# Optimization experiments

Measured on AMD Instinct MI355X. Metric: run time of the kernel, lower is better.

Reference implementation:

```python
import jax, jax.numpy as jnp
import numpy as np

HIDDEN = 128
HEADS = 8
HEAD_DIM = HIDDEN // HEADS
N = 2048
SCALE = HEAD_DIM ** -0.5


def setup_inputs() -> dict:
    key = jax.random.key(0)
    ks = jax.random.split(key, 12)
    # xavier_uniform bound for square (HIDDEN, HIDDEN) weights
    bound = float(np.sqrt(6.0 / (HIDDEN + HIDDEN)))
    def w(k):
        return jax.random.uniform(k, (HIDDEN, HIDDEN), jnp.float32, -bound, bound)
    return {
        "x": jax.random.normal(ks[0], (N, HIDDEN), jnp.float32),
        "attention_bias": jax.random.normal(ks[1], (N, N, HEADS), jnp.float32),
        "key_padding_mask": jnp.zeros((N,), jnp.bool_),
        "Wq": w(ks[2]), "bq": jnp.zeros((HIDDEN,), jnp.float32),
        "Wk": w(ks[3]), "bk": jnp.zeros((HIDDEN,), jnp.float32),
        "Wv": w(ks[4]), "bv": jnp.zeros((HIDDEN,), jnp.float32),
        "Wo": w(ks[5]), "bo": jnp.zeros((HIDDEN,), jnp.float32),
    }


def reference(x, attention_bias, key_padding_mask, Wq, bq, Wk, bk, Wv, bv, Wo, bo):
    n = x.shape[0]
    # torch Linear: y = x @ W.T + b
    q = (x @ Wq.T + bq).reshape(n, HEADS, HEAD_DIM).transpose(1, 0, 2)  # (H, N, D)
    k = (x @ Wk.T + bk).reshape(n, HEADS, HEAD_DIM).transpose(1, 0, 2)
    v = (x @ Wv.T + bv).reshape(n, HEADS, HEAD_DIM).transpose(1, 0, 2)
    scores = jnp.einsum('hnd,hmd->hnm', q, k) * SCALE        # (H, N, N)
    scores = scores + attention_bias.transpose(2, 0, 1)       # additive graph bias
    mask = key_padding_mask[None, None, :]                    # (1, 1, N) over keys
    scores = jnp.where(mask, -jnp.inf, scores)
    attn = jax.nn.softmax(scores, axis=-1)
    out = jnp.einsum('hnm,hmd->hnd', attn, v)                 # (H, N, D)
    out = out.transpose(1, 0, 2).reshape(n, HIDDEN)
    return out @ Wo.T + bo
```

## Files before the change

kernel.cpp:

```cpp
#include <hip/hip_runtime.h>
#include <hip/hip_bf16.h>

#define NSEQ 2048
#define HID 128
#define HEADS 8
#define HD 16
#define SCALE 0.25f
#define TQ 16
#define TK 64
#define SPLIT 8
#define KT_PER (NSEQ / TK / SPLIT)
#define QROW 160
#define PM_W 36
#define PH_W (16 * PM_W + 4)

typedef unsigned short ushort_t;
typedef __attribute__((ext_vector_type(8))) short short8;
typedef __attribute__((ext_vector_type(4))) float floatx4;

__device__ __forceinline__ void unpack2(unsigned u, float& a, float& b) {
    union { unsigned x; float f; } lo, hi;
    lo.x = u << 16; hi.x = u & 0xffff0000u;
    a = lo.f; b = hi.f;
}
__device__ __forceinline__ void unpack8(uint4 u, float* f) {
    unpack2(u.x, f[0], f[1]); unpack2(u.y, f[2], f[3]);
    unpack2(u.z, f[4], f[5]); unpack2(u.w, f[6], f[7]);
}
__device__ __forceinline__ unsigned pack_bf16x2(float a, float b) {
    __hip_bfloat16 ba = __float2bfloat16(a);
    __hip_bfloat16 bb = __float2bfloat16(b);
    return (unsigned)*(ushort_t*)&ba | ((unsigned)*(ushort_t*)&bb << 16);
}

__global__ __launch_bounds__(256) void transpose_kernel(
    const float* __restrict__ Wq, const float* __restrict__ Wk,
    const float* __restrict__ Wv, const float* __restrict__ Wo,
    float* __restrict__ wt)
{
    __shared__ float ts[32][33];
    const int mat = blockIdx.x >> 4, tile = blockIdx.x & 15;
    const int r0 = (tile >> 2) * 32, c0 = (tile & 3) * 32;
    const float* W = (mat == 0) ? Wq : (mat == 1) ? Wk : (mat == 2) ? Wv : Wo;
    const int lr = threadIdx.x >> 5;
    const int lc = threadIdx.x & 31;
#pragma unroll
    for (int i = 0; i < 4; ++i)
        ts[lr + i * 8][lc] = W[(r0 + lr + i * 8) * HID + c0 + lc];
    __syncthreads();
    float* dst = wt + mat * 16384;
#pragma unroll
    for (int i = 0; i < 4; ++i)
        dst[(c0 + lr + i * 8) * HID + r0 + lc] = ts[lc][lr + i * 8];
}

__global__ __launch_bounds__(128) void qkv_kernel(
    const float* __restrict__ x, const float* __restrict__ WqT,
    const float* __restrict__ WkT, const float* __restrict__ WvT,
    const float* __restrict__ bq, const float* __restrict__ bk,
    const float* __restrict__ bv, float* __restrict__ Qm,
    __hip_bfloat16* __restrict__ Kb, __hip_bfloat16* __restrict__ Vt)
{
    __shared__ float xs[4 * HID];
    const int j = threadIdx.x;
    const int mat = blockIdx.x >> 9;
    const int rb = blockIdx.x & 511;
    const int r0 = rb * 4;
    const float* WT = (mat == 0) ? WqT : (mat == 1) ? WkT : WvT;
    const float* bb = (mat == 0) ? bq : (mat == 1) ? bk : bv;
    ((float4*)xs)[j] = ((const float4*)(x + (size_t)r0 * HID))[j];
    __syncthreads();
    float acc[4];
#pragma unroll
    for (int r = 0; r < 4; ++r) acc[r] = 0.f;
#pragma unroll 8
    for (int i = 0; i < HID; ++i) {
        float w = WT[i * HID + j];
#pragma unroll
        for (int r = 0; r < 4; ++r) acc[r] = fmaf(xs[r * HID + i], w, acc[r]);
    }
    float bv_ = bb[j];
#pragma unroll
    for (int r = 0; r < 4; ++r) acc[r] += bv_;
    if (mat == 0) {
#pragma unroll
        for (int r = 0; r < 4; ++r) Qm[(size_t)(r0 + r) * HID + j] = acc[r];
    } else if (mat == 1) {
#pragma unroll
        for (int r = 0; r < 4; ++r) Kb[(size_t)(r0 + r) * HID + j] = __float2bfloat16(acc[r]);
    } else {
        unsigned u0 = pack_bf16x2(acc[0], acc[1]);
        unsigned u1 = pack_bf16x2(acc[2], acc[3]);
        *(uint2*)((ushort_t*)Vt + (size_t)j * NSEQ + r0) = make_uint2(u0, u1);
    }
}

__global__ __launch_bounds__(256, 4) void attn_kernel(
    const float* __restrict__ Qm, const __hip_bfloat16* __restrict__ Kb,
    const __hip_bfloat16* __restrict__ Vt, const float* __restrict__ bias,
    const unsigned char* __restrict__ mask, float* __restrict__ Op,
    float* __restrict__ Lp)
{
    __shared__ float qs[TQ * QROW];
    __shared__ float Pbuf[8 * PH_W];
    __shared__ float wl[4 * TQ * HEADS];

    const int t = threadIdx.x;
    const int lane = t & 63;
    const int wid = t >> 6;
    const int qb = blockIdx.x & 127;
    const int sp = blockIdx.x >> 7;
    const int n0 = qb * TQ;

    const int sc_mp = t >> 3;
    const int sc_h  = t & 7;
    const int kk = wid & 1;
    const int hbase = (wid >> 1) * 4;
    const int frag_m = lane & 15;
    const int frag_q = lane >> 4;

    {
        for (int idx = t; idx < 512; idx += 256) {
            int r = idx >> 5, c = idx & 31;
            int h = c >> 2, dg = c & 3;
            float4 v = ((const float4*)(Qm + (size_t)n0 * HID))[idx];
            *(float4*)&qs[r * QROW + h * 20 + dg * 4] = v;
        }
    }
    floatx4 acc[4];
#pragma unroll
    for (int hh = 0; hh < 4; ++hh) acc[hh] = (floatx4){0.f, 0.f, 0.f, 0.f};
    float lsum[TQ];
#pragma unroll
    for (int r = 0; r < TQ; ++r) lsum[r] = 0.0f;
    __syncthreads();

    for (int kt = 0; kt < KT_PER; ++kt) {
        const int m0 = (sp * KT_PER + kt) * TK;
        {
            const int m1 = m0 + sc_mp * 2;
            float bb0[TQ], bb1[TQ];
            const float* bp = bias + ((size_t)n0 * NSEQ + m1) * HEADS + sc_h;
#pragma unroll
            for (int r = 0; r < TQ; ++r) {
                bb0[r] = bp[(size_t)r * (NSEQ * HEADS)];
                bb1[r] = bp[(size_t)r * (NSEQ * HEADS) + HEADS];
            }
            const ushort_t* kp = (const ushort_t*)Kb + (size_t)m1 * HID + sc_h * HD;
            uint4 ka = *(const uint4*)kp;
            uint4 kb2 = *(const uint4*)(kp + 8);
            uint4 kc = *(const uint4*)(kp + HID);
            uint4 kd = *(const uint4*)(kp + HID + 8);
            float k0[16], k1[16];
            unpack8(ka, k0); unpack8(kb2, k0 + 8);
            unpack8(kc, k1); unpack8(kd, k1 + 8);
            const bool msk0 = mask[m1] != 0;
            const bool msk1 = mask[m1 + 1] != 0;
            unsigned* Pw = (unsigned*)Pbuf;
#pragma unroll
            for (int r = 0; r < TQ; ++r) {
                const float* qr = &qs[r * QROW + sc_h * 20];
                float qf[16];
                *(float4*)&qf[0]  = *(const float4*)(qr);
                *(float4*)&qf[4]  = *(const float4*)(qr + 4);
                *(float4*)&qf[8]  = *(const float4*)(qr + 8);
                *(float4*)&qf[12] = *(const float4*)(qr + 12);
                float d0 = 0.f, d1 = 0.f;
#pragma unroll
                for (int i = 0; i < 16; ++i) {
                    d0 = fmaf(qf[i], k0[i], d0);
                    d1 = fmaf(qf[i], k1[i], d1);
                }
                float s0 = fmaf(d0, SCALE, bb0[r]);
                float s1 = fmaf(d1, SCALE, bb1[r]);
                if (msk0) s0 = -INFINITY;
                if (msk1) s1 = -INFINITY;
                float e0 = __expf(s0);
                float e1 = __expf(s1);
                lsum[r] += e0 + e1;
                Pw[sc_h * PH_W + r * PM_W + sc_mp] = pack_bf16x2(e0, e1);
            }
        }
        __syncthreads();
        {
            const unsigned* Pw = (const unsigned*)Pbuf;
#pragma unroll
            for (int hh = 0; hh < 4; ++hh) {
                const int h = hbase + hh;
                const ushort_t* vrow = (const ushort_t*)Vt +
                    ((size_t)(h * HD + frag_m)) * NSEQ + m0 + kk * 32 + frag_q * 8;
                short8 bfrag = *(const short8*)vrow;
                short8 afrag = *(const short8*)&Pw[h * PH_W + frag_m * PM_W + kk * 16 + frag_q * 4];
                acc[hh] = __builtin_amdgcn_mfma_f32_16x16x32_bf16(afrag, bfrag, acc[hh], 0, 0, 0);
            }
        }
        __syncthreads();
    }

#pragma unroll
    for (int r = 0; r < TQ; ++r) {
        lsum[r] += __shfl_xor(lsum[r], 8);
        lsum[r] += __shfl_xor(lsum[r], 16);
        lsum[r] += __shfl_xor(lsum[r], 32);
    }
    if (lane < 8) {
#pragma unroll
        for (int r = 0; r < TQ; ++r)
            wl[wid * (TQ * HEADS) + r * 8 + lane] = lsum[r];
    }
    {
        float* obuf = Pbuf;
#pragma unroll
        for (int hh = 0; hh < 4; ++hh) {
#pragma unroll
            for (int reg = 0; reg < 4; ++reg) {
                int m = frag_q * 4 + reg;
                obuf[kk * 2048 + (hbase + hh) * 256 + m * 16 + frag_m] = acc[hh][reg];
            }
        }
    }
    __syncthreads();
    if (t < 128) {
        const float* obuf = Pbuf;
#pragma unroll
        for (int r = 0; r < TQ; ++r) {
            int h = t >> 4, d = t & 15;
            float v = obuf[h * 256 + r * 16 + d] + obuf[2048 + h * 256 + r * 16 + d];
            Op[((size_t)sp * NSEQ + n0 + r) * HID + t] = v;
        }
        const int r2 = t >> 3, h2 = t & 7;
        float l = wl[r2 * 8 + h2] + wl[128 + r2 * 8 + h2] +
                  wl[256 + r2 * 8 + h2] + wl[384 + r2 * 8 + h2];
        Lp[((size_t)sp * NSEQ + n0 + r2) * HEADS + h2] = l;
    }
}

__global__ __launch_bounds__(128) void proj_kernel(
    const float* __restrict__ Op, const float* __restrict__ Lp,
    const float* __restrict__ WoT, const float* __restrict__ bo,
    float* __restrict__ out)
{
    __shared__ float xs[2 * HID];
    const int j = threadIdx.x;
    const int r0 = blockIdx.x * 2;
    const int hh = j >> 4;
#pragma unroll
    for (int r = 0; r < 2; ++r) {
        const size_t n = r0 + r;
        float s = 0.f, l = 0.f;
#pragma unroll
        for (int sp = 0; sp < SPLIT; ++sp) {
            s += Op[((size_t)sp * NSEQ + n) * HID + j];
            l += Lp[((size_t)sp * NSEQ + n) * HEADS + hh];
        }
        xs[r * HID + j] = s / l;
    }
    __syncthreads();
    float acc[2];
    acc[0] = 0.f; acc[1] = 0.f;
#pragma unroll 8
    for (int i = 0; i < HID; ++i) {
        float w = WoT[i * HID + j];
        acc[0] = fmaf(xs[i], w, acc[0]);
        acc[1] = fmaf(xs[HID + i], w, acc[1]);
    }
    float b = bo[j];
    out[(size_t)r0 * HID + j] = acc[0] + b;
    out[(size_t)(r0 + 1) * HID + j] = acc[1] + b;
}

extern "C" void kernel_launch(void* const* d_in, const int* in_sizes, int n_in,
                              void* d_out, int out_size, void* d_ws, size_t ws_size,
                              hipStream_t stream) {
    const float* x    = (const float*)d_in[0];
    const float* bias = (const float*)d_in[1];
    const unsigned char* mask = (const unsigned char*)d_in[2];
    const float* Wq = (const float*)d_in[3];
    const float* bq = (const float*)d_in[4];
    const float* Wk = (const float*)d_in[5];
    const float* bk = (const float*)d_in[6];
    const float* Wv = (const float*)d_in[7];
    const float* bv = (const float*)d_in[8];
    const float* Wo = (const float*)d_in[9];
    const float* bo = (const float*)d_in[10];
    float* out = (float*)d_out;

    float* w = (float*)d_ws;
    float* WqT = w;
    float* WkT = w + 16384;
    float* WvT = w + 32768;
    float* WoT = w + 49152;
    float* Qm  = w + 65536;
    __hip_bfloat16* Kb = (__hip_bfloat16*)(w + 327680);
    __hip_bfloat16* Vt = (__hip_bfloat16*)(w + 458752);
    float* Op  = w + 589824;
    float* Lp  = w + 589824 + (size_t)SPLIT * NSEQ * HID;

    transpose_kernel<<<64, 256, 0, stream>>>(Wq, Wk, Wv, Wo, w);
    qkv_kernel<<<1536, 128, 0, stream>>>(x, WqT, WkT, WvT, bq, bk, bv, Qm, Kb, Vt);
    attn_kernel<<<128 * SPLIT, 256, 0, stream>>>(Qm, Kb, Vt, bias, mask, Op, Lp);
    proj_kernel<<<1024, 128, 0, stream>>>(Op, Lp, WoT, bo, out);
}
```

Before: 251.6 us.

## Store Q/K as fp16, use fdot2 for scores, prefetch bias next tile

Q and K are now written as fp16 by the projection kernel, and the attention score loop uses packed fp16 dot products (fdot2) instead of unpacking bf16 into fp32 FMAs. The bias loads for the next key tile are issued before the current tile's compute to hide global latency. Mask values are hoisted out of the loop, and the kernel-tile loop is fully unrolled. This cuts ALU work and LDS traffic for Q, but rounding Q to fp16 reduces precision, and the extra bias registers raise register pressure.

```diff
diff --git a/kernel.cpp b/kernel.cpp
--- a/kernel.cpp
+++ b/kernel.cpp
@@ -10,27 +10,37 @@
 #define TK 64
 #define SPLIT 8
 #define KT_PER (NSEQ / TK / SPLIT)
-#define QROW 160
+#define QROW_H 68
 #define PM_W 36
 #define PH_W (16 * PM_W + 4)
 
 typedef unsigned short ushort_t;
 typedef __attribute__((ext_vector_type(8))) short short8;
 typedef __attribute__((ext_vector_type(4))) float floatx4;
-
-__device__ __forceinline__ void unpack2(unsigned u, float& a, float& b) {
-    union { unsigned x; float f; } lo, hi;
-    lo.x = u << 16; hi.x = u & 0xffff0000u;
-    a = lo.f; b = hi.f;
-}
-__device__ __forceinline__ void unpack8(uint4 u, float* f) {
-    unpack2(u.x, f[0], f[1]); unpack2(u.y, f[2], f[3]);
-    unpack2(u.z, f[4], f[5]); unpack2(u.w, f[6], f[7]);
-}
+typedef _Float16 half2_t __attribute__((ext_vector_type(2)));
+
+#if __has_builtin(__builtin_amdgcn_fdot2)
+#define FDOT2(a, b, c) __builtin_amdgcn_fdot2((a), (b), (c), false)
+#else
+__device__ __forceinline__ float FDOT2(half2_t a, half2_t b, float c) {
+    return fmaf((float)a[0], (float)b[0], fmaf((float)a[1], (float)b[1], c));
+}
+#endif
+
 __device__ __forceinline__ unsigned pack_bf16x2(float a, float b) {
     __hip_bfloat16 ba = __float2bfloat16(a);
     __hip_bfloat16 bb = __float2bfloat16(b);
     return (unsigned)*(ushort_t*)&ba | ((unsigned)*(ushort_t*)&bb << 16);
+}
+__device__ __forceinline__ unsigned pack_f16x2(float a, float b) {
+    _Float16 ha = (_Float16)a, hb = (_Float16)b;
+    return (unsigned)*(ushort_t*)&ha | ((unsigned)*(ushort_t*)&hb << 16);
+}
+__device__ __forceinline__ void ld_h8(const void* p, half2_t* d) {
+    uint4 v = *(const uint4*)p;
+    union { unsigned u; half2_t h; } c;
+    c.u = v.x; d[0] = c.h; c.u = v.y; d[1] = c.h;
+    c.u = v.z; d[2] = c.h; c.u = v.w; d[3] = c.h;
 }
 
 __global__ __launch_bounds__(256) void transpose_kernel(
@@ -58,8 +68,8 @@
     const float* __restrict__ x, const float* __restrict__ WqT,
     const float* __restrict__ WkT, const float* __restrict__ WvT,
     const float* __restrict__ bq, const float* __restrict__ bk,
-    const float* __restrict__ bv, float* __restrict__ Qm,
-    __hip_bfloat16* __restrict__ Kb, __hip_bfloat16* __restrict__ Vt)
+    const float* __restrict__ bv, ushort_t* __restrict__ Qh,
+    ushort_t* __restrict__ Kh, __hip_bfloat16* __restrict__ Vt)
 {
     __shared__ float xs[4 * HID];
     const int j = threadIdx.x;
@@ -83,11 +93,18 @@
 #pragma unroll
     for (int r = 0; r < 4; ++r) acc[r] += bv_;
     if (mat == 0) {
-#pragma unroll
-        for (int r = 0; r < 4; ++r) Qm[(size_t)(r0 + r) * HID + j] = acc[r];
+        ushort_t* dst = Qh;
+#pragma unroll
+        for (int r = 0; r < 4; ++r) {
+            _Float16 h = (_Float16)acc[r];
+            dst[(size_t)(r0 + r) * HID + j] = *(ushort_t*)&h;
+        }
     } else if (mat == 1) {
 #pragma unroll
-        for (int r = 0; r < 4; ++r) Kb[(size_t)(r0 + r) * HID + j] = __float2bfloat16(acc[r]);
+        for (int r = 0; r < 4; ++r) {
+            _Float16 h = (_Float16)acc[r];
+            Kh[(size_t)(r0 + r) * HID + j] = *(ushort_t*)&h;
+        }
     } else {
         unsigned u0 = pack_bf16x2(acc[0], acc[1]);
         unsigned u1 = pack_bf16x2(acc[2], acc[3]);
@@ -96,12 +113,12 @@
 }
 
 __global__ __launch_bounds__(256, 4) void attn_kernel(
-    const float* __restrict__ Qm, const __hip_bfloat16* __restrict__ Kb,
+    const ushort_t* __restrict__ Qh, const ushort_t* __restrict__ Kh,
     const __hip_bfloat16* __restrict__ Vt, const float* __restrict__ bias,
     const unsigned char* __restrict__ mask, float* __restrict__ Op,
     float* __restrict__ Lp)
 {
-    __shared__ float qs[TQ * QROW];
+    __shared__ unsigned qs[TQ * QROW_H];
     __shared__ float Pbuf[8 * PH_W];
     __shared__ float wl[4 * TQ * HEADS];
 
@@ -119,13 +136,29 @@
     const int frag_m = lane & 15;
     const int frag_q = lane >> 4;
 
+    const float* bp_base = bias + ((size_t)n0 * NSEQ + sc_mp * 2) * HEADS + sc_h;
+    const size_t m_base = (size_t)(sp * KT_PER) * TK;
+
+    float cb0[TQ], cb1[TQ];
     {
-        for (int idx = t; idx < 512; idx += 256) {
-            int r = idx >> 5, c = idx & 31;
-            int h = c >> 2, dg = c & 3;
-            float4 v = ((const float4*)(Qm + (size_t)n0 * HID))[idx];
-            *(float4*)&qs[r * QROW + h * 20 + dg * 4] = v;
-        }
+        const float* bp = bp_base + m_base * HEADS;
+#pragma unroll
+        for (int r = 0; r < TQ; ++r) {
+            cb0[r] = bp[(size_t)r * (NSEQ * HEADS)];
+            cb1[r] = bp[(size_t)r * (NSEQ * HEADS) + HEADS];
+        }
+    }
+    bool mk0[KT_PER], mk1[KT_PER];
+#pragma unroll
+    for (int kt = 0; kt < KT_PER; ++kt) {
+        const size_t m1 = m_base + kt * TK + sc_mp * 2;
+        mk0[kt] = mask[m1] != 0;
+        mk1[kt] = mask[m1 + 1] != 0;
+    }
+    {
+        const int qr = t >> 4, qc = t & 15;
+        uint4 v = *(const uint4*)(Qh + (size_t)(n0 + qr) * HID + qc * 8);
+        *(uint4*)&qs[qr * QROW_H + qc * 4] = v;
     }
     floatx4 acc[4];
 #pragma unroll
@@ -135,44 +168,40 @@
     for (int r = 0; r < TQ; ++r) lsum[r] = 0.0f;
     __syncthreads();
 
+#pragma unroll
     for (int kt = 0; kt < KT_PER; ++kt) {
-        const int m0 = (sp * KT_PER + kt) * TK;
+        const size_t m0 = m_base + kt * TK;
+        half2_t k0[8], k1[8];
         {
-            const int m1 = m0 + sc_mp * 2;
-            float bb0[TQ], bb1[TQ];
-            const float* bp = bias + ((size_t)n0 * NSEQ + m1) * HEADS + sc_h;
+            const ushort_t* kp = Kh + (m0 + sc_mp * 2) * HID + sc_h * HD;
+            ld_h8(kp, k0); ld_h8(kp + 8, k0 + 4);
+            ld_h8(kp + HID, k1); ld_h8(kp + HID + 8, k1 + 4);
+        }
+        float nb0[TQ], nb1[TQ];
+        if (kt + 1 < KT_PER) {
+            const float* bp = bp_base + (m_base + (kt + 1) * TK) * HEADS;
 #pragma unroll
             for (int r = 0; r < TQ; ++r) {
-                bb0[r] = bp[(size_t)r * (NSEQ * HEADS)];
-                bb1[r] = bp[(size_t)r * (NSEQ * HEADS) + HEADS];
+                nb0[r] = bp[(size_t)r * (NSEQ * HEADS)];
+                nb1[r] = bp[(size_t)r * (NSEQ * HEADS) + HEADS];
             }
-            const ushort_t* kp = (const ushort_t*)Kb + (size_t)m1 * HID + sc_h * HD;
-            uint4 ka = *(const uint4*)kp;
-            uint4 kb2 = *(const uint4*)(kp + 8);
-            uint4 kc = *(const uint4*)(kp + HID);
-            uint4 kd = *(const uint4*)(kp + HID + 8);
-            float k0[16], k1[16];
-            unpack8(ka, k0); unpack8(kb2, k0 + 8);
-            unpack8(kc, k1); unpack8(kd, k1 + 8);
-            const bool msk0 = mask[m1] != 0;
-            const bool msk1 = mask[m1 + 1] != 0;
+        }
+        {
+            const bool msk0 = mk0[kt], msk1 = mk1[kt];
             unsigned* Pw = (unsigned*)Pbuf;
 #pragma unroll
             for (int r = 0; r < TQ; ++r) {
-                const float* qr = &qs[r * QROW + sc_h * 20];
-                float qf[16];
-                *(float4*)&qf[0]  = *(const float4*)(qr);
-                *(float4*)&qf[4]  = *(const float4*)(qr + 4);
-                *(float4*)&qf[8]  = *(const float4*)(qr + 8);
-                *(float4*)&qf[12] = *(const float4*)(qr + 12);
+                half2_t qf[8];
+                const unsigned* qw = &qs[r * QROW_H + sc_h * 8];
+                ld_h8(qw, qf); ld_h8(qw + 4, qf + 4);
                 float d0 = 0.f, d1 = 0.f;
 #pragma unroll
-                for (int i = 0; i < 16; ++i) {
-                    d0 = fmaf(qf[i], k0[i], d0);
-                    d1 = fmaf(qf[i], k1[i], d1);
+                for (int i = 0; i < 8; ++i) {
+                    d0 = FDOT2(qf[i], k0[i], d0);
+                    d1 = FDOT2(qf[i], k1[i], d1);
                 }
-                float s0 = fmaf(d0, SCALE, bb0[r]);
-                float s1 = fmaf(d1, SCALE, bb1[r]);
+                float s0 = fmaf(d0, SCALE, cb0[r]);
+                float s1 = fmaf(d1, SCALE, cb1[r]);
                 if (msk0) s0 = -INFINITY;
                 if (msk1) s1 = -INFINITY;
                 float e0 = __expf(s0);
@@ -195,6 +224,10 @@
             }
         }
         __syncthreads();
+        if (kt + 1 < KT_PER) {
+#pragma unroll
+            for (int r = 0; r < TQ; ++r) { cb0[r] = nb0[r]; cb1[r] = nb1[r]; }
+        }
     }
 
 #pragma unroll
@@ -290,14 +323,14 @@
     float* WkT = w + 16384;
     float* WvT = w + 32768;
     float* WoT = w + 49152;
-    float* Qm  = w + 65536;
-    __hip_bfloat16* Kb = (__hip_bfloat16*)(w + 327680);
-    __hip_bfloat16* Vt = (__hip_bfloat16*)(w + 458752);
-    float* Op  = w + 589824;
-    float* Lp  = w + 589824 + (size_t)SPLIT * NSEQ * HID;
+    ushort_t* Qh = (ushort_t*)(w + 65536);
+    ushort_t* Kh = (ushort_t*)(w + 196608);
+    __hip_bfloat16* Vt = (__hip_bfloat16*)(w + 327680);
+    float* Op  = w + 458752;
+    float* Lp  = w + 458752 + (size_t)SPLIT * NSEQ * HID;
 
     transpose_kernel<<<64, 256, 0, stream>>>(Wq, Wk, Wv, Wo, w);
-    qkv_kernel<<<1536, 128, 0, stream>>>(x, WqT, WkT, WvT, bq, bk, bv, Qm, Kb, Vt);
-    attn_kernel<<<128 * SPLIT, 256, 0, stream>>>(Qm, Kb, Vt, bias, mask, Op, Lp);
+    qkv_kernel<<<1536, 128, 0, stream>>>(x, WqT, WkT, WvT, bq, bk, bv, Qh, Kh, Vt);
+    attn_kernel<<<128 * SPLIT, 256, 0, stream>>>(Qh, Kh, Vt, bias, mask, Op, Lp);
     proj_kernel<<<1024, 128, 0, stream>>>(Op, Lp, WoT, bo, out);
 }
```

Result: slower. 285.2 us (+13.3%).
